# Kernel optimization log

Measured on AMD Instinct MI355X. Metric: run time of the kernel, lower is better.

The kernel has to match this reference:

```python
import jax, jax.numpy as jnp
import numpy as np

T = 64    # target_len
D = 256   # av_dim


def setup_inputs() -> dict:
    key = jax.random.key(0)
    ks = jax.random.split(key, 8)
    B, L = 128, 512
    return {
        "acoustic_seq": jax.random.normal(ks[0], (B, L, D), jnp.float32),
        "visual_seq": jax.random.normal(ks[1], (B, L, D), jnp.float32),
        "IS_BAG_list": jnp.ones((B, L), jnp.int32),
        # h_fc: Linear(target_len, target_len)
        "Wh": jax.random.normal(ks[2], (T, T), jnp.float32) * 0.05,
        "bh": jax.random.normal(ks[3], (T,), jnp.float32) * 0.05,
        # w_fc: Linear(av_dim, av_dim)
        "Ww": jax.random.normal(ks[4], (D, D), jnp.float32) * 0.05,
        "bw": jax.random.normal(ks[5], (D,), jnp.float32) * 0.05,
        # conv: Conv2d(2, 1, kernel_size=1) -> two scalars + bias
        "conv_w": jax.random.normal(ks[6], (2,), jnp.float32) * 0.5,
        "conv_b": jax.random.normal(ks[7], (1,), jnp.float32) * 0.1,
    }


def reference(acoustic_seq, visual_seq, IS_BAG_list, Wh, bh, Ww, bw, conv_w, conv_b):
    B, L, Dd = acoustic_seq.shape
    G = L // T  # uniform group size (deterministic variant of random group sizes)
    mapping = jnp.repeat(jnp.arange(T), G)  # [L] pooled-frame index per original frame

    # resize_sequence (m_len > target_len branch): group-mean pooling to T frames
    aco_p = acoustic_seq.reshape(B, T, G, Dd).mean(axis=2)  # [B,T,D]
    vis_p = visual_seq.reshape(B, T, G, Dd).mean(axis=2)    # [B,T,D]

    # c_attention = sigmoid(Conv2d(2->1, 1x1)(stack([aco,vis], ch)))
    c_att = jax.nn.sigmoid(conv_w[0] * aco_p + conv_w[1] * vis_p + conv_b[0])  # [B,T,D]

    # hw_attention = mean over channel dim
    hw = 0.5 * (aco_p + vis_p)                                 # [B,T,D]
    h_att = jax.nn.sigmoid(hw.mean(axis=2) @ Wh.T + bh)        # [B,T]
    w_att = jax.nn.sigmoid(hw.mean(axis=1) @ Ww.T + bw)        # [B,D]

    # recover_sequence (m_len > target_len): gather attention[mapping]
    h_full = h_att[:, mapping][..., None]   # [B,L,1]
    w_full = w_att[:, None, :]              # [B,1,D]
    c_full = c_att[:, mapping, :]           # [B,L,D]

    scale = (h_full + w_full + c_full) / 3.0
    mask = (IS_BAG_list == 1)[..., None]    # [B,L,1]
    aco_out = jnp.where(mask, acoustic_seq * scale, acoustic_seq)
    vis_out = jnp.where(mask, visual_seq * scale, visual_seq)
    return aco_out, vis_out
```

## Files before the change

kernel.cpp:

```cpp
#include <hip/hip_runtime.h>
#include <math.h>

#define BB 128
#define LL 512
#define DD 256
#define TT 64
#define GG 8

__device__ __forceinline__ float sigm(float x) {
    return 1.0f / (1.0f + __expf(-x));
}

__global__ void k_pool(const float* __restrict__ aco, const float* __restrict__ vis,
                       const float* __restrict__ conv_w, const float* __restrict__ conv_b,
                       float* __restrict__ c_att, float* __restrict__ hw_buf,
                       float* __restrict__ hwRowMean)
{
    const int bt = blockIdx.x;
    const int d  = threadIdx.x;
    const int b  = bt >> 6;
    const int t  = bt & 63;

    size_t base = ((size_t)(b * LL + t * GG)) * DD + d;
    float sa = 0.f, sv = 0.f;
#pragma unroll
    for (int g = 0; g < GG; ++g) {
        sa += aco[base + (size_t)g * DD];
        sv += vis[base + (size_t)g * DD];
    }
    sa *= (1.0f / GG);
    sv *= (1.0f / GG);

    const float cw0 = conv_w[0], cw1 = conv_w[1], cb = conv_b[0];
    const float hw = 0.5f * (sa + sv);

    c_att[(size_t)bt * DD + d]  = sigm(cw0 * sa + cw1 * sv + cb);
    hw_buf[(size_t)bt * DD + d] = hw;

    __shared__ float red[DD];
    red[d] = hw;
    __syncthreads();
    for (int s = DD / 2; s > 0; s >>= 1) {
        if (d < s) red[d] += red[d + s];
        __syncthreads();
    }
    if (d == 0) hwRowMean[bt] = red[0] * (1.0f / DD);
}

__global__ void k_hatt(const float* __restrict__ hwRowMean, const float* __restrict__ Wh,
                       const float* __restrict__ bh, float* __restrict__ h_att)
{
    const int b = blockIdx.x;
    const int t = threadIdx.x;
    __shared__ float row[TT];
    row[t] = hwRowMean[b * TT + t];
    __syncthreads();
    float s = bh[t];
#pragma unroll
    for (int j = 0; j < TT; ++j) s += row[j] * Wh[t * TT + j];
    h_att[b * TT + t] = sigm(s);
}

__global__ void k_watt(const float* __restrict__ hw_buf, const float* __restrict__ Ww,
                       const float* __restrict__ bw, float* __restrict__ w_att)
{
    const int b = blockIdx.x;
    const int d = threadIdx.x;
    float s = 0.f;
    const float* hb = hw_buf + (size_t)b * TT * DD + d;
#pragma unroll
    for (int t = 0; t < TT; ++t) s += hb[(size_t)t * DD];

    __shared__ float cm[DD];
    cm[d] = s * (1.0f / TT);
    __syncthreads();

    float acc = bw[d];
    const float* wr = Ww + (size_t)d * DD;
#pragma unroll 4
    for (int k = 0; k < DD; k += 4) {
        float4 w4 = *reinterpret_cast<const float4*>(wr + k);
        acc += cm[k] * w4.x + cm[k + 1] * w4.y + cm[k + 2] * w4.z + cm[k + 3] * w4.w;
    }
    w_att[b * DD + d] = sigm(acc);
}

__global__ void k_apply(const float* __restrict__ aco, const float* __restrict__ vis,
                        const int* __restrict__ isbag,
                        const float* __restrict__ c_att, const float* __restrict__ h_att,
                        const float* __restrict__ w_att,
                        float* __restrict__ out)
{
    const size_t N4 = (size_t)BB * LL * DD / 4;
    size_t i = (size_t)blockIdx.x * blockDim.x + threadIdx.x;
    if (i >= N4) return;

    const int row = (int)(i >> 6);
    const int dq  = (int)(i & 63);
    const int b   = row >> 9;
    const int l   = row & 511;
    const int t   = l >> 3;

    const float h  = h_att[b * TT + t];
    const float4 w4 = *reinterpret_cast<const float4*>(w_att + b * DD + dq * 4);
    const float4 c4 = *reinterpret_cast<const float4*>(c_att + ((size_t)(b * TT + t)) * DD + dq * 4);
    const bool  m  = (isbag[row] == 1);

    const float4 a4 = reinterpret_cast<const float4*>(aco)[i];
    const float4 v4 = reinterpret_cast<const float4*>(vis)[i];

    const float inv3 = 1.0f / 3.0f;
    float4 s4;
    s4.x = (h + w4.x + c4.x) * inv3;
    s4.y = (h + w4.y + c4.y) * inv3;
    s4.z = (h + w4.z + c4.z) * inv3;
    s4.w = (h + w4.w + c4.w) * inv3;

    float4 oa, ov;
    oa.x = m ? a4.x * s4.x : a4.x;
    oa.y = m ? a4.y * s4.y : a4.y;
    oa.z = m ? a4.z * s4.z : a4.z;
    oa.w = m ? a4.w * s4.w : a4.w;
    ov.x = m ? v4.x * s4.x : v4.x;
    ov.y = m ? v4.y * s4.y : v4.y;
    ov.z = m ? v4.z * s4.z : v4.z;
    ov.w = m ? v4.w * s4.w : v4.w;

    reinterpret_cast<float4*>(out)[i]      = oa;
    reinterpret_cast<float4*>(out)[N4 + i] = ov;
}

extern "C" void kernel_launch(void* const* d_in, const int* in_sizes, int n_in,
                              void* d_out, int out_size, void* d_ws, size_t ws_size,
                              hipStream_t stream) {
    const float* aco = (const float*)d_in[0];
    const float* vis = (const float*)d_in[1];
    const int*   isb = (const int*)d_in[2];
    const float* Wh  = (const float*)d_in[3];
    const float* bh  = (const float*)d_in[4];
    const float* Ww  = (const float*)d_in[5];
    const float* bw  = (const float*)d_in[6];
    const float* cw  = (const float*)d_in[7];
    const float* cb  = (const float*)d_in[8];
    float* out = (float*)d_out;

    float* ws = (float*)d_ws;
    float* c_att     = ws;
    float* hw_buf    = c_att  + (size_t)BB * TT * DD;
    float* hwRowMean = hw_buf + (size_t)BB * TT * DD;
    float* h_att     = hwRowMean + BB * TT;
    float* w_att     = h_att + BB * TT;

    k_pool<<<BB * TT, DD, 0, stream>>>(aco, vis, cw, cb, c_att, hw_buf, hwRowMean);
    k_hatt<<<BB, TT, 0, stream>>>(hwRowMean, Wh, bh, h_att);
    k_watt<<<BB, DD, 0, stream>>>(hw_buf, Ww, bw, w_att);

    const size_t N4 = (size_t)BB * LL * DD / 4;
    k_apply<<<(int)(N4 / 256), 256, 0, stream>>>(aco, vis, isb, c_att, h_att, w_att, out);
}
```

Measured before the change: 81.20 us.

## Vectorize pooling, fuse gate kernels, grid-stride apply with nontemporal stores

The pooling kernel now handles four (b,t) rows per block, each wavefront loading float4 vectors, and replaces the shared-memory tree reduction with wave shuffles. The h and w gate kernels are merged into one launch, removing a kernel boundary. The apply kernel becomes a grid-stride loop over 2048 blocks and writes its outputs with nontemporal stores to cut cache pollution. The main aim is lower launch overhead and better memory throughput on a bandwidth-bound workload. In exchange, each apply thread runs more loop iterations, and the nontemporal hints may behave differently on this hardware.

```diff
diff --git a/kernel.cpp b/kernel.cpp
--- a/kernel.cpp
+++ b/kernel.cpp
@@ -7,127 +7,117 @@
 #define TT 64
 #define GG 8
 
+typedef float f32x4 __attribute__((ext_vector_type(4)));
+
 __device__ __forceinline__ float sigm(float x) {
     return 1.0f / (1.0f + __expf(-x));
 }
 
-__global__ void k_pool(const float* __restrict__ aco, const float* __restrict__ vis,
+__global__ void k_pool(const f32x4* __restrict__ aco, const f32x4* __restrict__ vis,
                        const float* __restrict__ conv_w, const float* __restrict__ conv_b,
-                       float* __restrict__ c_att, float* __restrict__ hw_buf,
+                       f32x4* __restrict__ c_att, f32x4* __restrict__ hw_buf,
                        float* __restrict__ hwRowMean)
 {
-    const int bt = blockIdx.x;
-    const int d  = threadIdx.x;
-    const int b  = bt >> 6;
-    const int t  = bt & 63;
+    const int tid = threadIdx.x;
+    const int q   = tid & 63;
+    const int r   = tid >> 6;
+    const int bt  = blockIdx.x * 4 + r;
+    const int b   = bt >> 6;
+    const int t   = bt & 63;
 
-    size_t base = ((size_t)(b * LL + t * GG)) * DD + d;
-    float sa = 0.f, sv = 0.f;
+    size_t base = ((size_t)(b * LL + t * GG)) * (DD / 4) + q;
+    f32x4 sa = 0.f, sv = 0.f;
 #pragma unroll
     for (int g = 0; g < GG; ++g) {
-        sa += aco[base + (size_t)g * DD];
-        sv += vis[base + (size_t)g * DD];
+        sa += aco[base + (size_t)g * (DD / 4)];
+        sv += vis[base + (size_t)g * (DD / 4)];
     }
-    sa *= (1.0f / GG);
-    sv *= (1.0f / GG);
+    sa *= 0.125f;
+    sv *= 0.125f;
 
     const float cw0 = conv_w[0], cw1 = conv_w[1], cb = conv_b[0];
-    const float hw = 0.5f * (sa + sv);
+    f32x4 z  = cw0 * sa + cw1 * sv + cb;
+    f32x4 ca;
+    ca.x = sigm(z.x); ca.y = sigm(z.y); ca.z = sigm(z.z); ca.w = sigm(z.w);
+    f32x4 hw = 0.5f * (sa + sv);
 
-    c_att[(size_t)bt * DD + d]  = sigm(cw0 * sa + cw1 * sv + cb);
-    hw_buf[(size_t)bt * DD + d] = hw;
+    c_att[(size_t)bt * (DD / 4) + q]  = ca;
+    hw_buf[(size_t)bt * (DD / 4) + q] = hw;
 
-    __shared__ float red[DD];
-    red[d] = hw;
-    __syncthreads();
-    for (int s = DD / 2; s > 0; s >>= 1) {
-        if (d < s) red[d] += red[d + s];
-        __syncthreads();
-    }
-    if (d == 0) hwRowMean[bt] = red[0] * (1.0f / DD);
+    float hsum = hw.x + hw.y + hw.z + hw.w;
+#pragma unroll
+    for (int off = 32; off > 0; off >>= 1)
+        hsum += __shfl_xor(hsum, off, 64);
+    if (q == 0) hwRowMean[bt] = hsum * (1.0f / DD);
 }
 
-__global__ void k_hatt(const float* __restrict__ hwRowMean, const float* __restrict__ Wh,
-                       const float* __restrict__ bh, float* __restrict__ h_att)
-{
-    const int b = blockIdx.x;
-    const int t = threadIdx.x;
-    __shared__ float row[TT];
-    row[t] = hwRowMean[b * TT + t];
-    __syncthreads();
-    float s = bh[t];
-#pragma unroll
-    for (int j = 0; j < TT; ++j) s += row[j] * Wh[t * TT + j];
-    h_att[b * TT + t] = sigm(s);
-}
-
-__global__ void k_watt(const float* __restrict__ hw_buf, const float* __restrict__ Ww,
-                       const float* __restrict__ bw, float* __restrict__ w_att)
+__global__ void k_gates(const float* __restrict__ hw_buf, const float* __restrict__ hwRowMean,
+                        const float* __restrict__ Wh, const float* __restrict__ bh,
+                        const float* __restrict__ Ww, const float* __restrict__ bw,
+                        float* __restrict__ h_att, float* __restrict__ w_att)
 {
     const int b = blockIdx.x;
     const int d = threadIdx.x;
+
+    __shared__ float row[TT];
+    __shared__ float cm[DD];
+
+    if (d < TT) row[d] = hwRowMean[b * TT + d];
+
     float s = 0.f;
     const float* hb = hw_buf + (size_t)b * TT * DD + d;
 #pragma unroll
     for (int t = 0; t < TT; ++t) s += hb[(size_t)t * DD];
-
-    __shared__ float cm[DD];
     cm[d] = s * (1.0f / TT);
     __syncthreads();
+
+    if (d < TT) {
+        float acc = bh[d];
+#pragma unroll
+        for (int j = 0; j < TT; ++j) acc += row[j] * Wh[d * TT + j];
+        h_att[b * TT + d] = sigm(acc);
+    }
 
     float acc = bw[d];
     const float* wr = Ww + (size_t)d * DD;
 #pragma unroll 4
     for (int k = 0; k < DD; k += 4) {
-        float4 w4 = *reinterpret_cast<const float4*>(wr + k);
+        f32x4 w4 = *reinterpret_cast<const f32x4*>(wr + k);
         acc += cm[k] * w4.x + cm[k + 1] * w4.y + cm[k + 2] * w4.z + cm[k + 3] * w4.w;
     }
     w_att[b * DD + d] = sigm(acc);
 }
 
-__global__ void k_apply(const float* __restrict__ aco, const float* __restrict__ vis,
+__global__ void k_apply(const f32x4* __restrict__ aco, const f32x4* __restrict__ vis,
                         const int* __restrict__ isbag,
-                        const float* __restrict__ c_att, const float* __restrict__ h_att,
-                        const float* __restrict__ w_att,
-                        float* __restrict__ out)
+                        const f32x4* __restrict__ c_att, const float* __restrict__ h_att,
+                        const f32x4* __restrict__ w_att,
+                        f32x4* __restrict__ out)
 {
     const size_t N4 = (size_t)BB * LL * DD / 4;
-    size_t i = (size_t)blockIdx.x * blockDim.x + threadIdx.x;
-    if (i >= N4) return;
+    const size_t stride = (size_t)gridDim.x * blockDim.x;
+    for (size_t i = (size_t)blockIdx.x * blockDim.x + threadIdx.x; i < N4; i += stride) {
+        const int row = (int)(i >> 6);
+        const int dq  = (int)(i & 63);
+        const int b   = row >> 9;
+        const int l   = row & 511;
+        const int t   = l >> 3;
 
-    const int row = (int)(i >> 6);
-    const int dq  = (int)(i & 63);
-    const int b   = row >> 9;
-    const int l   = row & 511;
-    const int t   = l >> 3;
+        const float h  = h_att[b * TT + t];
+        const f32x4 w4 = w_att[b * (DD / 4) + dq];
+        const f32x4 c4 = c_att[((size_t)(b * TT + t)) * (DD / 4) + dq];
+        const bool  m  = (isbag[row] == 1);
 
-    const float h  = h_att[b * TT + t];
-    const float4 w4 = *reinterpret_cast<const float4*>(w_att + b * DD + dq * 4);
-    const float4 c4 = *reinterpret_cast<const float4*>(c_att + ((size_t)(b * TT + t)) * DD + dq * 4);
-    const bool  m  = (isbag[row] == 1);
+        f32x4 a4 = aco[i];
+        f32x4 v4 = vis[i];
+        f32x4 s4 = (h + w4 + c4) * (1.0f / 3.0f);
 
-    const float4 a4 = reinterpret_cast<const float4*>(aco)[i];
-    const float4 v4 = reinterpret_cast<const float4*>(vis)[i];
+        f32x4 oa = m ? (f32x4)(a4 * s4) : a4;
+        f32x4 ov = m ? (f32x4)(v4 * s4) : v4;
 
-    const float inv3 = 1.0f / 3.0f;
-    float4 s4;
-    s4.x = (h + w4.x + c4.x) * inv3;
-    s4.y = (h + w4.y + c4.y) * inv3;
-    s4.z = (h + w4.z + c4.z) * inv3;
-    s4.w = (h + w4.w + c4.w) * inv3;
-
-    float4 oa, ov;
-    oa.x = m ? a4.x * s4.x : a4.x;
-    oa.y = m ? a4.y * s4.y : a4.y;
-    oa.z = m ? a4.z * s4.z : a4.z;
-    oa.w = m ? a4.w * s4.w : a4.w;
-    ov.x = m ? v4.x * s4.x : v4.x;
-    ov.y = m ? v4.y * s4.y : v4.y;
-    ov.z = m ? v4.z * s4.z : v4.z;
-    ov.w = m ? v4.w * s4.w : v4.w;
-
-    reinterpret_cast<float4*>(out)[i]      = oa;
-    reinterpret_cast<float4*>(out)[N4 + i] = ov;
+        __builtin_nontemporal_store(oa, &out[i]);
+        __builtin_nontemporal_store(ov, &out[N4 + i]);
+    }
 }
 
 extern "C" void kernel_launch(void* const* d_in, const int* in_sizes, int n_in,
@@ -151,10 +141,14 @@
     float* h_att     = hwRowMean + BB * TT;
     float* w_att     = h_att + BB * TT;
 
-    k_pool<<<BB * TT, DD, 0, stream>>>(aco, vis, cw, cb, c_att, hw_buf, hwRowMean);
-    k_hatt<<<BB, TT, 0, stream>>>(hwRowMean, Wh, bh, h_att);
-    k_watt<<<BB, DD, 0, stream>>>(hw_buf, Ww, bw, w_att);
+    k_pool<<<BB * TT / 4, 256, 0, stream>>>(
+        (const f32x4*)aco, (const f32x4*)vis, cw, cb,
+        (f32x4*)c_att, (f32x4*)hw_buf, hwRowMean);
 
-    const size_t N4 = (size_t)BB * LL * DD / 4;
-    k_apply<<<(int)(N4 / 256), 256, 0, stream>>>(aco, vis, isb, c_att, h_att, w_att, out);
+    k_gates<<<BB, DD, 0, stream>>>(hw_buf, hwRowMean, Wh, bh, Ww, bw, h_att, w_att);
+
+    k_apply<<<2048, 256, 0, stream>>>(
+        (const f32x4*)aco, (const f32x4*)vis, isb,
+        (const f32x4*)c_att, h_att, (const f32x4*)w_att,
+        (f32x4*)out);
 }
```

Measured after the change: 82.02 us. About the same (+1.0%).
